# Performance work log

Measured on AMD Instinct MI355X. Metric: run time of the kernel, lower is better.

Reference implementation:

```python
import jax, jax.numpy as jnp
import numpy as np

N_LAYERS = 2
D = 128


def _prelu(z, a):
    return jnp.where(z >= 0, z, a * z)


def _seg_sum(vals, idx, num):
    return jax.ops.segment_sum(vals, idx, num_segments=num)


def _conv_layer(x, ni, ei, Wn2e, bn2e, We2n, be2n, alpha, Dn_inv, De_inv, num_nodes, num_edges):
    # node -> edge: mean over member nodes (row norm), then linear + bias + PReLU
    e = _seg_sum((x @ Wn2e)[ni] * De_inv[ei][:, None], ei, num_edges) + bn2e
    e = _prelu(e, alpha)
    # edge -> node: mean over incident hyperedges
    n = _seg_sum((e @ We2n)[ei] * Dn_inv[ni][:, None], ni, num_nodes) + be2n
    return n, e


def _encoder(x, ni, ei, Wn2e, bn2e, We2n, be2n, alpha, Dn_inv, De_inv, num_nodes, num_edges):
    e = None
    for i in range(N_LAYERS):
        x, e = _conv_layer(x, ni, ei, Wn2e[i], bn2e[i], We2n[i], be2n[i], alpha, Dn_inv, De_inv, num_nodes, num_edges)
        x = _prelu(x, alpha)
    return x, e


def _decoder(x, e, ni, ei, We, Wx, b, alpha, Dn_inv, num_nodes):
    for i in range(N_LAYERS):
        m = _seg_sum((e @ We[i])[ei] * Dn_inv[ni][:, None], ni, num_nodes)
        x = _prelu(x @ Wx[i] + m + b[i], alpha)
    return x


def _forward(x, xx,
             e1_Wn2e, e1_bn2e, e1_We2n, e1_be2n,
             e2_Wn2e, e2_bn2e, e2_We2n, e2_be2n,
             d1_We, d1_Wx, d1_b, d2_We, d2_Wx, d2_b,
             alpha, node_idx, edge_idx, num_nodes, num_edges):
    # self loops: each node gets its own private hyperedge (id num_edges + node_id)
    ni = jnp.concatenate([node_idx, jnp.arange(num_nodes, dtype=node_idx.dtype)])
    ei = jnp.concatenate([edge_idx, jnp.arange(num_edges, num_edges + num_nodes, dtype=edge_idx.dtype)])
    ne_tot = num_edges + num_nodes
    ones = jnp.ones(ni.shape[0], x.dtype)
    Dn = _seg_sum(ones, ni, num_nodes)
    De = _seg_sum(ones, ei, ne_tot)
    Dn_inv = jnp.where(Dn > 0, 1.0 / Dn, 0.0)
    De_inv = jnp.where(De > 0, 1.0 / De, 0.0)

    n1, e1 = _encoder(x, ni, ei, e1_Wn2e, e1_bn2e, e1_We2n, e1_be2n, alpha, Dn_inv, De_inv, num_nodes, ne_tot)
    n2, e2 = _encoder(xx, ni, ei, e2_Wn2e, e2_bn2e, e2_We2n, e2_be2n, alpha, Dn_inv, De_inv, num_nodes, ne_tot)

    x11 = _decoder(n1, e1, ni, ei, d1_We, d1_Wx, d1_b, alpha, Dn_inv, num_nodes)
    x21 = _decoder(n2, e2, ni, ei, d2_We, d2_Wx, d2_b, alpha, Dn_inv, num_nodes)
    x12 = _decoder(n2, e2, ni, ei, d1_We, d1_Wx, d1_b, alpha, Dn_inv, num_nodes)
    x22 = _decoder(n1, e1, ni, ei, d2_We, d2_Wx, d2_b, alpha, Dn_inv, num_nodes)

    nn1 = jnp.concatenate([n1, n2], axis=1)
    return (nn1, n1, e1[:num_edges], n2, e2[:num_edges], x11, x21, x12, x22)


def setup_inputs() -> dict:
    key = jax.random.key(0)
    ks = jax.random.split(key, 24)
    N, E, NNZ = 50000, 20000, 800000
    s = 1.0 / np.sqrt(D)
    inp = {
        'x': jax.random.normal(ks[0], (N, D), jnp.float32),
        'xx': jax.random.normal(ks[1], (N, D), jnp.float32),
        'node_idx': jax.random.randint(ks[2], (NNZ,), 0, N, jnp.int32),
        'edge_idx': jax.random.randint(ks[3], (NNZ,), 0, E, jnp.int32),
        'num_nodes': N,
        'num_edges': E,
        'alpha': jnp.float32(0.25),
    }
    i = 4
    for enc in ('e1', 'e2'):
        inp[enc + '_Wn2e'] = jax.random.normal(ks[i], (N_LAYERS, D, D), jnp.float32) * s; i += 1
        inp[enc + '_bn2e'] = jnp.zeros((N_LAYERS, D), jnp.float32)
        inp[enc + '_We2n'] = jax.random.normal(ks[i], (N_LAYERS, D, D), jnp.float32) * s; i += 1
        inp[enc + '_be2n'] = jnp.zeros((N_LAYERS, D), jnp.float32)
    for dec in ('d1', 'd2'):
        inp[dec + '_We'] = jax.random.normal(ks[i], (N_LAYERS, D, D), jnp.float32) * s; i += 1
        inp[dec + '_Wx'] = jax.random.normal(ks[i], (N_LAYERS, D, D), jnp.float32) * s; i += 1
        inp[dec + '_b'] = jnp.zeros((N_LAYERS, D), jnp.float32)
    return inp


def reference(x, xx,
              e1_Wn2e, e1_bn2e, e1_We2n, e1_be2n,
              e2_Wn2e, e2_bn2e, e2_We2n, e2_be2n,
              d1_We, d1_Wx, d1_b, d2_We, d2_Wx, d2_b,
              alpha, node_idx, edge_idx, num_nodes, num_edges):
    return _forward(x, xx,
                    e1_Wn2e, e1_bn2e, e1_We2n, e1_be2n,
                    e2_Wn2e, e2_bn2e, e2_We2n, e2_be2n,
                    d1_We, d1_Wx, d1_b, d2_We, d2_Wx, d2_b,
                    alpha, node_idx, edge_idx, num_nodes, num_edges)
```

## Files before the change

kernel.cpp:

```cpp
#include <hip/hip_runtime.h>

#define DD 128

typedef __attribute__((ext_vector_type(8))) short bh8;
typedef __attribute__((ext_vector_type(8))) unsigned short us8;
typedef __attribute__((ext_vector_type(4))) float f4;
typedef unsigned int u32;
typedef unsigned short u16;

__device__ __forceinline__ u16 tob(float f) {
  u32 u = __builtin_bit_cast(u32, f);
  u += 0x7FFFu + ((u >> 16) & 1u);
  return (u16)(u >> 16);
}
__device__ __forceinline__ float fb(u16 h) { return __builtin_bit_cast(float, (u32)h << 16); }


__global__ __launch_bounds__(256) void init_counts_k(int* cn, int* ce, int N, int E) {
  int g = blockIdx.x * blockDim.x + threadIdx.x;
  if (g < E) ce[g] = 0;
  if (g < N) cn[g] = 0;
}


__global__ __launch_bounds__(256) void scan_partials_k(const int* __restrict__ cn, const int* __restrict__ ce,
                                                       int* part, int NCHN, int N, int NCHE, int E) {
  __shared__ int red[256];
  int b = blockIdx.x, tid = threadIdx.x;
  const int* cnt = (b < NCHN) ? cn : ce;
  int n = (b < NCHN) ? N : E;
  int base = ((b < NCHN) ? b : (b - NCHN)) << 10;
  int i0 = base + tid * 4;
  int s = 0;
  #pragma unroll
  for (int j = 0; j < 4; ++j) { int i = i0 + j; if (i < n) s += cnt[i]; }
  red[tid] = s; __syncthreads();
  for (int off = 128; off > 0; off >>= 1) {
    if (tid < off) red[tid] += red[tid + off];
    __syncthreads();
  }
  if (tid == 0) part[b] = red[0];
}

__device__ __forceinline__ int blk_excl_scan(int s, int tid, int* sums) {
  sums[tid] = s; __syncthreads();
  for (int off = 1; off < 256; off <<= 1) {
    int t = (tid >= off) ? sums[tid - off] : 0;
    __syncthreads();
    sums[tid] += t;
    __syncthreads();
  }
  int ex = sums[tid] - s;
  __syncthreads();
  return ex;
}

__global__ __launch_bounds__(256) void scan_apply_k(const int* __restrict__ cn, const int* __restrict__ ce,
                                                    const int* __restrict__ part,
                                                    int* offs_n, int* offs_e,
                                                    int NCHN, int N, int NCHE, int E) {
  __shared__ int sums[256];
  __shared__ int base_s;
  int b = blockIdx.x, tid = threadIdx.x;
  const bool isN = b < NCHN;
  const int* cnt = isN ? cn : ce;
  int* offs = isN ? offs_n : offs_e;
  int n = isN ? N : E;
  int nch = isN ? NCHN : NCHE;
  int c = isN ? b : b - NCHN;
  const int* pbase = isN ? part : part + NCHN;
  {
    int v = (tid < nch) ? pbase[tid] : 0;
    int ex = blk_excl_scan(v, tid, sums);
    if (tid == c) base_s = ex;
  }
  __syncthreads();
  int base = (c << 10);
  int i0 = base + tid * 4;
  int v[4]; int s = 0;
  #pragma unroll
  for (int j = 0; j < 4; ++j) { int i = i0 + j; int t = (i < n) ? cnt[i] : 0; v[j] = t; s += t; }
  int ex = blk_excl_scan(s, tid, sums);
  int run = base_s + ex;
  #pragma unroll
  for (int j = 0; j < 4; ++j) { int i = i0 + j; if (i < n) offs[i] = run; run += v[j]; }
  if (tid == 255 && base + 1024 >= n) offs[n] = run;
}

__global__ __launch_bounds__(256) void fill_deg_k(const int* __restrict__ offs_n, const int* __restrict__ offs_e,
                                                  float* Dn_inv, float* De_inv,
                                                  int* cur_be, int* cur_bn,
                                                  int N, int E, int NBE, int NBN) {
  int g = blockIdx.x * blockDim.x + threadIdx.x;
  if (g < E) {
    int b = offs_e[g], e = offs_e[g + 1];
    De_inv[g] = (e > b) ? 1.0f / (float)(e - b) : 0.0f;
  }
  if (g < N) {
    int b = offs_n[g], e = offs_n[g + 1];
    Dn_inv[g] = 1.0f / (float)(e - b + 1);
  }
  if (g < NBE) {
    int r1 = (g + 1) * 32; if (r1 > E) r1 = E;
    int o0 = offs_e[g * 32], o1 = offs_e[r1];
    int C = o1 - o0, base = 8 * o0;
    #pragma unroll
    for (int k = 0; k < 8; ++k) cur_be[g * 8 + k] = base + k * C;
  }
  if (g < NBN) {
    int r1 = (g + 1) * 32; if (r1 > N) r1 = N;
    int o0 = offs_n[g * 32], o1 = offs_n[r1];
    int C = o1 - o0, base = 8 * o0;
    #pragma unroll
    for (int k = 0; k < 8; ++k) cur_bn[g * 8 + k] = base + k * C;
  }
}

__global__ __launch_bounds__(256) void partition2_k(const int* __restrict__ ni, const int* __restrict__ ei,
                                                    int* cur_be, int* cur_bn,
                                                    u32* __restrict__ SE, u32* __restrict__ SN, int nnz) {
  int xcd;
  asm volatile("s_getreg_b32 %0, hwreg(HW_REG_XCC_ID)" : "=s"(xcd));
  xcd &= 7;
  int stride = gridDim.x * blockDim.x;
  for (int j = blockIdx.x * blockDim.x + threadIdx.x; j < nnz; j += stride) {
    int n = ni[j], e = ei[j];
    int pe = atomicAdd(&cur_be[(e >> 5) * 8 + xcd], 1);
    SE[pe] = ((u32)(e & 31) << 17) | (u32)n;
    int pn = atomicAdd(&cur_bn[(n >> 5) * 8 + xcd], 1);
    SN[pn] = ((u32)(n & 31) << 17) | (u32)e;
  }
}

__device__ __forceinline__ void scatter_body(const u32* __restrict__ S, const int* __restrict__ offs,
                                             const int* __restrict__ cur_b,
                                             int* __restrict__ list, int nRows, int b, int tid, int* cur) {
  const int i0 = b << 5;
  if (tid < 32) {
    int row = i0 + tid;
    cur[tid] = (row < nRows) ? offs[row] : 0;
  }
  __syncthreads();
  int r1 = i0 + 32; if (r1 > nRows) r1 = nRows;
  const int o0 = offs[i0];
  const int C = offs[r1] - o0;
  #pragma unroll 1
  for (int k = 0; k < 8; ++k) {
    int sbeg = 8 * o0 + k * C;
    int send = cur_b[b * 8 + k];
    for (int i = sbeg + tid; i < send; i += 256) {
      u32 v = S[i];
      int pos = atomicAdd(&cur[v >> 17], 1);
      list[pos] = (int)(v & 0x1FFFFu);
    }
  }
}

__global__ __launch_bounds__(256) void scatter_both_k(const u32* SE, const int* offs_e, const int* cur_be,
                                                      int* listE, int E, int NBE,
                                                      const u32* SN, const int* offs_n, const int* cur_bn,
                                                      int* listN, int N) {
  __shared__ int cur[32];
  int b = blockIdx.x, tid = threadIdx.x;
  if (b < NBE) scatter_body(SE, offs_e, cur_be, listE, E, b, tid, cur);
  else         scatter_body(SN, offs_n, cur_bn, listN, N, b - NBE, tid, cur);
}


__device__ __forceinline__ void acc8(float a[8], us8 v) {
  #pragma unroll
  for (int j = 0; j < 8; ++j) a[j] += fb(v[j]);
}

template<int SPLIT>
__global__ __launch_bounds__(256) void gather_edge_k(const u16* __restrict__ srcb,
                                                     const int* __restrict__ offs, const int* __restrict__ list,
                                                     const float* __restrict__ De_inv,
                                                     const float* __restrict__ b1, const float* __restrict__ b2,
                                                     const float* __restrict__ alphap,
                                                     u16* __restrict__ e_fullb,
                                                     float* __restrict__ d2a, float* __restrict__ d2b, int E) {
  const int wave = threadIdx.x >> 6, lane = threadIdx.x & 63;
  const int row = blockIdx.x * 4 + wave;
  if (row >= E) return;
  const int half = lane >> 5, cl = lane & 31;
  const int c8 = cl * 8;
  const int beg = offs[row], end = offs[row + 1];
  float a0[8] = {0,0,0,0,0,0,0,0}, a1[8] = {0,0,0,0,0,0,0,0};
  int i = beg + half;
  for (; i + 2 < end; i += 4) {
    us8 v0 = *(const us8*)&srcb[(size_t)list[i] * 256 + c8];
    us8 v1 = *(const us8*)&srcb[(size_t)list[i + 2] * 256 + c8];
    acc8(a0, v0); acc8(a1, v1);
  }
  if (i < end) acc8(a0, *(const us8*)&srcb[(size_t)list[i] * 256 + c8]);
  float s[8];
  #pragma unroll
  for (int j = 0; j < 8; ++j) s[j] = a0[j] + a1[j];
  #pragma unroll
  for (int j = 0; j < 8; ++j) s[j] += __shfl_xor(s[j], 32);
  if (half == 0) {
    float sc = De_inv[row];
    const float* bp = (c8 < 128) ? (b1 + c8) : (b2 + c8 - 128);
    float4 bt0 = *(const float4*)bp;
    float4 bt1 = *(const float4*)(bp + 4);
    float bb[8] = {bt0.x, bt0.y, bt0.z, bt0.w, bt1.x, bt1.y, bt1.z, bt1.w};
    float al = *alphap;
    us8 ob;
    float ov[8];
    #pragma unroll
    for (int j = 0; j < 8; ++j) {
      float v = sc * s[j] + bb[j];
      v = (v >= 0.f) ? v : al * v;
      ov[j] = v; ob[j] = tob(v);
    }
    *(us8*)&e_fullb[(size_t)row * 256 + c8] = ob;
    if constexpr (SPLIT == 1) {
      float* dp = (c8 < 128) ? &d2a[(size_t)row * DD + c8] : &d2b[(size_t)row * DD + c8 - 128];
      float4 w0 = {ov[0], ov[1], ov[2], ov[3]};
      float4 w1 = {ov[4], ov[5], ov[6], ov[7]};
      *(float4*)dp = w0;
      *(float4*)(dp + 4) = w1;
    }
  }
}

__global__ __launch_bounds__(256) void gather_node_k(const u16* __restrict__ e_fullb,
                                                     const u16* __restrict__ tb,
                                                     const int* __restrict__ offs, const int* __restrict__ list,
                                                     const float* __restrict__ Dn_inv,
                                                     const float* __restrict__ b1, const float* __restrict__ b2,
                                                     const float* __restrict__ alphap,
                                                     u16* __restrict__ dstb, int N) {
  const int wave = threadIdx.x >> 6, lane = threadIdx.x & 63;
  const int row = blockIdx.x * 4 + wave;
  if (row >= N) return;
  const int half = lane >> 5, cl = lane & 31;
  const int c8 = cl * 8;
  const int beg = offs[row], end = offs[row + 1];
  float a0[8] = {0,0,0,0,0,0,0,0}, a1[8] = {0,0,0,0,0,0,0,0};
  int i = beg + half;
  for (; i + 2 < end; i += 4) {
    us8 v0 = *(const us8*)&e_fullb[(size_t)list[i] * 256 + c8];
    us8 v1 = *(const us8*)&e_fullb[(size_t)list[i + 2] * 256 + c8];
    acc8(a0, v0); acc8(a1, v1);
  }
  if (i < end) acc8(a0, *(const us8*)&e_fullb[(size_t)list[i] * 256 + c8]);
  float s[8];
  #pragma unroll
  for (int j = 0; j < 8; ++j) s[j] = a0[j] + a1[j];
  #pragma unroll
  for (int j = 0; j < 8; ++j) s[j] += __shfl_xor(s[j], 32);
  if (half == 0) {
    us8 tv = *(const us8*)&tb[(size_t)row * 256 + c8];
    const float* bp = (c8 < 128) ? (b1 + c8) : (b2 + c8 - 128);
    float4 bt0 = *(const float4*)bp;
    float4 bt1 = *(const float4*)(bp + 4);
    float bb[8] = {bt0.x, bt0.y, bt0.z, bt0.w, bt1.x, bt1.y, bt1.z, bt1.w};
    float al = *alphap;
    float sc = Dn_inv[row];
    us8 ob;
    #pragma unroll
    for (int j = 0; j < 8; ++j) {
      float sv = fb(tv[j]) + bb[j];
      sv = (sv >= 0.f) ? sv : al * sv;
      ob[j] = tob(sc * (sv + s[j]));
    }
    *(us8*)&dstb[(size_t)row * 256 + c8] = ob;
  }
}


struct WPtrs { const float* p[16]; };

__global__ __launch_bounds__(256) void prep_w_k(WPtrs wp, char* dst) {
  int m = blockIdx.x >> 3, s = blockIdx.x & 7;
  const float* W = wp.p[m];
  int t = threadIdx.x;
  int n = t & 127;
  int k0 = s * 16 + (t >> 7) * 8;
  us8 vhi, vlo;
  #pragma unroll
  for (int j = 0; j < 8; ++j) {
    float x = W[(size_t)(k0 + j) * DD + n];
    u32 ux = __builtin_bit_cast(u32, x);
    float hf = __builtin_bit_cast(float, ux & 0xFFFF0000u);
    float l = x - hf;
    vhi[j] = (u16)(ux >> 16);
    vlo[j] = (u16)(__builtin_bit_cast(u32, l) >> 16);
  }
  char* base = dst + (size_t)m * 65536;
  int byte = n * 256 + k0 * 2;
  byte ^= (n & 7) << 4;
  *(us8*)(base + byte) = vhi;
  *(us8*)(base + 32768 + byte) = vlo;
}


__device__ __forceinline__ void stage_w(const char* gsrc, char* lds, int tid) {
  int wave = tid >> 6, lane = tid & 63;
  #pragma unroll
  for (int i = 0; i < 16; ++i) {
    int off = (wave * 16 + i) * 1024;
    __builtin_amdgcn_global_load_lds(
        (const __attribute__((address_space(1))) u32*)(gsrc + off + lane * 16),
        (__attribute__((address_space(3))) u32*)(lds + off), 16, 0, 0);
  }
}

__device__ __forceinline__ void split8(const float vs[8], bh8& hi, bh8& lo) {
  #pragma unroll
  for (int j = 0; j < 8; ++j) {
    u32 u = __builtin_bit_cast(u32, vs[j]);
    float hf = __builtin_bit_cast(float, u & 0xFFFF0000u);
    float l = vs[j] - hf;
    hi[j] = (short)(u >> 16);
    lo[j] = (short)(__builtin_bit_cast(u32, l) >> 16);
  }
}

__device__ __forceinline__ void mk_afrag(const float* rowp, int koff, bh8& hi, bh8& lo) {
  float4 v0 = *(const float4*)(rowp + koff);
  float4 v1 = *(const float4*)(rowp + koff + 4);
  float vs[8] = {v0.x, v0.y, v0.z, v0.w, v1.x, v1.y, v1.z, v1.w};
  split8(vs, hi, lo);
}

__device__ __forceinline__ void mfma_ks(const bh8& ahi, const bh8& alo, const char* Wl,
                                        int ks, int lane, f4 acc[8]) {
  const int koff0 = (lane >> 4) * 8;
  const int k2 = (ks * 32 + koff0) * 2;
  #pragma unroll
  for (int cb = 0; cb < 8; ++cb) {
    int n = cb * 16 + (lane & 15);
    int byte = (n * 256 + k2) ^ ((n & 7) << 4);
    bh8 bhiF = *(const bh8*)(Wl + byte);
    bh8 bloF = *(const bh8*)(Wl + 32768 + byte);
    acc[cb] = __builtin_amdgcn_mfma_f32_16x16x32_bf16(ahi, bhiF, acc[cb], 0, 0, 0);
    acc[cb] = __builtin_amdgcn_mfma_f32_16x16x32_bf16(ahi, bloF, acc[cb], 0, 0, 0);
    acc[cb] = __builtin_amdgcn_mfma_f32_16x16x32_bf16(alo, bhiF, acc[cb], 0, 0, 0);
  }
}

__device__ __forceinline__ void mfma_ks_bf(const bh8& a, const char* Wl,
                                           int ks, int lane, f4 acc[8]) {
  const int koff0 = (lane >> 4) * 8;
  const int k2 = (ks * 32 + koff0) * 2;
  #pragma unroll
  for (int cb = 0; cb < 8; ++cb) {
    int n = cb * 16 + (lane & 15);
    int byte = (n * 256 + k2) ^ ((n & 7) << 4);
    bh8 bhiF = *(const bh8*)(Wl + byte);
    bh8 bloF = *(const bh8*)(Wl + 32768 + byte);
    acc[cb] = __builtin_amdgcn_mfma_f32_16x16x32_bf16(a, bhiF, acc[cb], 0, 0, 0);
    acc[cb] = __builtin_amdgcn_mfma_f32_16x16x32_bf16(a, bloF, acc[cb], 0, 0, 0);
  }
}

__device__ __forceinline__ void mfma_passS(const float* __restrict__ A, size_t astride, int acoff,
                                           const char* Wl, int rbase, int nrows, int lane, f4 acc[8]) {
  int r = rbase + (lane & 15);
  if (r >= nrows) r = nrows - 1;
  const float* rowp = A + (size_t)r * astride + acoff;
  const int koff0 = (lane >> 4) * 8;
  #pragma unroll
  for (int ks = 0; ks < 4; ++ks) {
    bh8 ahi, alo;
    mk_afrag(rowp, ks * 32 + koff0, ahi, alo);
    mfma_ks(ahi, alo, Wl, ks, lane, acc);
  }
}

__device__ __forceinline__ void mfma_passB(const u16* __restrict__ A, size_t astride, int acoff,
                                           const char* Wl, int rbase, int nrows, int lane, f4 acc[8]) {
  int r = rbase + (lane & 15);
  if (r >= nrows) r = nrows - 1;
  const u16* rowp = A + (size_t)r * astride + acoff;
  const int koff0 = (lane >> 4) * 8;
  #pragma unroll
  for (int ks = 0; ks < 4; ++ks) {
    bh8 a = __builtin_bit_cast(bh8, *(const us8*)(rowp + ks * 32 + koff0));
    mfma_ks_bf(a, Wl, ks, lane, acc);
  }
}

struct AFragB { bh8 a[4]; };

__device__ __forceinline__ void load_afragB(const u16* __restrict__ A, size_t astride, int acoff,
                                            int rbase, int nrows, int lane, AFragB& f) {
  int r = rbase + (lane & 15);
  if (r >= nrows) r = nrows - 1;
  const u16* rowp = A + (size_t)r * astride + acoff;
  const int koff0 = (lane >> 4) * 8;
  #pragma unroll
  for (int ks = 0; ks < 4; ++ks)
    f.a[ks] = __builtin_bit_cast(bh8, *(const us8*)(rowp + ks * 32 + koff0));
}

__device__ __forceinline__ void mfma_pass_fragB(const AFragB& f, const char* Wl, int lane, f4 acc[8]) {
  #pragma unroll
  for (int ks = 0; ks < 4; ++ks) mfma_ks_bf(f.a[ks], Wl, ks, lane, acc);
}


__device__ __forceinline__ void acc_to_T(f4 acc[8], const float* bias, float al,
                                         char* Tb, int wave, int lane) {
  const int cidx = lane & 15;
  float b8[8];
  #pragma unroll
  for (int cb = 0; cb < 8; ++cb) b8[cb] = bias[cb * 16 + cidx];
  #pragma unroll
  for (int q = 0; q < 4; ++q) {
    int row = wave * 16 + (lane >> 4) * 4 + q;
    #pragma unroll
    for (int cb = 0; cb < 8; ++cb) {
      float v = acc[cb][q] + b8[cb];
      v = (v >= 0.f) ? v : al * v;
      int byte = (row * 256 + (cb * 16 + cidx) * 2) ^ ((row & 7) << 4);
      *(u16*)(Tb + byte) = tob(v);
    }
  }
}

__device__ __forceinline__ void load_fT(const char* Tb, int wave, int lane, AFragB& f) {
  const int row = wave * 16 + (lane & 15);
  const int koff0 = (lane >> 4) * 8;
  #pragma unroll
  for (int ks = 0; ks < 4; ++ks) {
    int byte = (row * 256 + (ks * 32 + koff0) * 2) ^ ((row & 7) << 4);
    f.a[ks] = __builtin_bit_cast(bh8, *(const us8*)(Tb + byte));
  }
}

template<int MODE, int OBF>
__device__ __forceinline__ void epilogueS(f4 acc[8], const float* bias, const float* alphap,
                                          void* outp, size_t ostride, int ocoff,
                                          int rbase, int nrows, int lane) {
  float al = 0.f;
  if constexpr (MODE == 1) al = *alphap;
  const int cidx = lane & 15;
  int rq = rbase + (lane >> 4) * 4;
  float b8[8];
  if constexpr (MODE == 1) {
    #pragma unroll
    for (int cb = 0; cb < 8; ++cb) b8[cb] = bias[cb * 16 + cidx];
  }
  #pragma unroll
  for (int q = 0; q < 4; ++q) {
    int row = rq + q;
    if (row < nrows) {
      #pragma unroll
      for (int cb = 0; cb < 8; ++cb) {
        float v = acc[cb][q];
        if constexpr (MODE == 1) { v += b8[cb]; v = (v >= 0.f) ? v : al * v; }
        if constexpr (OBF == 1) {
          u16* op = (u16*)outp + (size_t)row * ostride + ocoff + cidx;
          op[cb * 16] = tob(v);
        } else {
          float* op = (float*)outp + (size_t)row * ostride + ocoff + cidx;
          op[cb * 16] = v;
        }
      }
    }
  }
}

#define ACC_ZERO(acc) { _Pragma("unroll") for (int cb = 0; cb < 8; ++cb) acc[cb] = {0.f, 0.f, 0.f, 0.f}; }


__global__ __launch_bounds__(256, 2) void combo1_k(const float* __restrict__ x, const char* W0,
                                                   const float* __restrict__ xx, const char* W4,
                                                   u16* __restrict__ tb, int nrows, int NT,
                                                   const int* __restrict__ ni, const int* __restrict__ ei,
                                                   int* cn, int* ce, int nnz) {
  __shared__ char Wl[65536];
  if ((int)blockIdx.x < NT) {
    const int wave = threadIdx.x >> 6, lane = threadIdx.x & 63;
    const int rbase = blockIdx.x * 64 + wave * 16;
    f4 acc[8];
    stage_w(W0, Wl, threadIdx.x);
    __syncthreads();
    ACC_ZERO(acc);
    mfma_passS(x, DD, 0, Wl, rbase, nrows, lane, acc);
    epilogueS<0, 1>(acc, nullptr, nullptr, tb, 256, 0, rbase, nrows, lane);
    __syncthreads();
    stage_w(W4, Wl, threadIdx.x);
    __syncthreads();
    ACC_ZERO(acc);
    mfma_passS(xx, DD, 0, Wl, rbase, nrows, lane, acc);
    epilogueS<0, 1>(acc, nullptr, nullptr, tb, 256, 128, rbase, nrows, lane);
  } else {
    int nb = gridDim.x - NT;
    int stride = nb * 256;
    for (int j = ((int)blockIdx.x - NT) * 256 + (int)threadIdx.x; j < nnz; j += stride) {
      atomicAdd(&cn[ni[j]], 1);
      atomicAdd(&ce[ei[j]], 1);
    }
  }
}

__global__ __launch_bounds__(256, 2) void gemm_fuse_hid_k(const u16* __restrict__ thb,
                                                          const char* W20, const float* b20, const char* W21,
                                                          const char* W60, const float* b60, const char* W61,
                                                          const float* __restrict__ alphap,
                                                          u16* __restrict__ tb_out, int nrows) {
  __shared__ char Wl[65536];
  const int wave = threadIdx.x >> 6, lane = threadIdx.x & 63;
  const int rbase = blockIdx.x * 64 + wave * 16;
  const float al = *alphap;
  f4 acc[8];
  AFragB fT;
  #pragma unroll 1
  for (int h = 0; h < 2; ++h) {
    if (h) __syncthreads();
    stage_w(h ? W60 : W20, Wl, threadIdx.x);
    __syncthreads();
    ACC_ZERO(acc);
    mfma_passB(thb, 256, h * 128, Wl, rbase, nrows, lane, acc);
    __syncthreads();
    acc_to_T(acc, h ? b60 : b20, al, Wl, wave, lane);
    __syncthreads();
    load_fT(Wl, wave, lane, fT);
    __syncthreads();
    stage_w(h ? W61 : W21, Wl, threadIdx.x);
    __syncthreads();
    ACC_ZERO(acc);
    mfma_pass_fragB(fT, Wl, lane, acc);
    epilogueS<0, 1>(acc, nullptr, nullptr, tb_out, 256, h * 128, rbase, nrows, lane);
  }
}

__global__ __launch_bounds__(256, 2) void enc_final_k(const u16* __restrict__ aggb, const char* W1, const float* b1_,
                                                      const char* W2, const float* b2_,
                                                      const float* __restrict__ alphap,
                                                      float* __restrict__ n1, float* __restrict__ n2,
                                                      u16* __restrict__ n1b, u16* __restrict__ n2b,
                                                      float* __restrict__ nn1, int nrows) {
  __shared__ char Wl[65536];
  const int wave = threadIdx.x >> 6, lane = threadIdx.x & 63;
  const int rbase = blockIdx.x * 64 + wave * 16;
  const int cidx = lane & 15;
  f4 acc[8];
  float al = *alphap;
  #pragma unroll 1
  for (int h = 0; h < 2; ++h) {
    if (h) __syncthreads();
    stage_w(h ? W2 : W1, Wl, threadIdx.x);
    __syncthreads();
    const float* bp = h ? b2_ : b1_;
    float* nout = h ? n2 : n1;
    u16* nbout = h ? n2b : n1b;
    float b8[8];
    #pragma unroll
    for (int cb = 0; cb < 8; ++cb) b8[cb] = bp[cb * 16 + cidx];
    ACC_ZERO(acc);
    mfma_passB(aggb, 256, h * 128, Wl, rbase, nrows, lane, acc);
    int rq = rbase + (lane >> 4) * 4;
    #pragma unroll
    for (int q = 0; q < 4; ++q) {
      int row = rq + q;
      if (row < nrows) {
        float* op = nout + (size_t)row * DD + cidx;
        float* op2 = nn1 + (size_t)row * 256 + h * 128 + cidx;
        u16* op3 = nbout + (size_t)row * DD + cidx;
        #pragma unroll
        for (int cb = 0; cb < 8; ++cb) {
          float v = acc[cb][q] + b8[cb];
          v = (v >= 0.f) ? v : al * v;
          op[cb * 16] = v;
          op2[cb * 16] = v;
          op3[cb * 16] = tob(v);
        }
      }
    }
  }
}

__global__ __launch_bounds__(256, 2) void dec_fused_k(const u16* __restrict__ n1b, const u16* __restrict__ n2b,
                                                      const u16* __restrict__ aggb,
                                                      const char* Wx10, const char* We10, const float* b1_0,
                                                      const char* Wx11, const char* We11, const float* b1_1,
                                                      const char* Wx20, const char* We20, const float* b2_0,
                                                      const char* Wx21, const char* We21, const float* b2_1,
                                                      const float* __restrict__ alphap,
                                                      float* __restrict__ x11, float* __restrict__ x22,
                                                      float* __restrict__ x12, float* __restrict__ x21,
                                                      int nrows) {
  __shared__ char Wl[65536];
  const int y = blockIdx.y;
  const u16* xb = y ? n2b : n1b;
  float* od1 = y ? x12 : x11;
  float* od2 = y ? x21 : x22;
  const int acoff = y * 128;
  const int wave = threadIdx.x >> 6, lane = threadIdx.x & 63;
  const int rbase = blockIdx.x * 64 + wave * 16;
  const float al = *alphap;
  AFragB fx, fa, fT;
  load_afragB(xb, DD, 0, rbase, nrows, lane, fx);
  load_afragB(aggb, 256, acoff, rbase, nrows, lane, fa);
  f4 acc[8];
  #pragma unroll 1
  for (int s = 0; s < 2; ++s) {
    const char* Wx0 = s ? Wx20 : Wx10;
    const char* We0 = s ? We20 : We10;
    const char* Wx1 = s ? Wx21 : Wx11;
    const char* We1 = s ? We21 : We11;
    const float* b0 = s ? b2_0 : b1_0;
    const float* b1 = s ? b2_1 : b1_1;
    float* out = s ? od2 : od1;
    if (s) __syncthreads();
    stage_w(Wx0, Wl, threadIdx.x);
    __syncthreads();
    ACC_ZERO(acc);
    mfma_pass_fragB(fx, Wl, lane, acc);
    __syncthreads();
    stage_w(We0, Wl, threadIdx.x);
    __syncthreads();
    mfma_pass_fragB(fa, Wl, lane, acc);
    __syncthreads();
    acc_to_T(acc, b0, al, Wl, wave, lane);
    __syncthreads();
    load_fT(Wl, wave, lane, fT);
    __syncthreads();
    stage_w(Wx1, Wl, threadIdx.x);
    __syncthreads();
    ACC_ZERO(acc);
    mfma_pass_fragB(fT, Wl, lane, acc);
    __syncthreads();
    stage_w(We1, Wl, threadIdx.x);
    __syncthreads();
    mfma_pass_fragB(fa, Wl, lane, acc);
    epilogueS<1, 0>(acc, b1, alphap, out, DD, 0, rbase, nrows, lane);
  }
}


extern "C" void kernel_launch(void* const* d_in, const int* in_sizes, int n_in,
                              void* d_out, int out_size, void* d_ws, size_t ws_size,
                              hipStream_t stream) {
  const float* x        = (const float*)d_in[0];
  const float* xx       = (const float*)d_in[1];
  const int*   node_idx = (const int*)d_in[2];
  const int*   edge_idx = (const int*)d_in[3];
  const float* alphap   = (const float*)d_in[6];
  const float* e1_Wn2e  = (const float*)d_in[7];
  const float* e1_bn2e  = (const float*)d_in[8];
  const float* e1_We2n  = (const float*)d_in[9];
  const float* e1_be2n  = (const float*)d_in[10];
  const float* e2_Wn2e  = (const float*)d_in[11];
  const float* e2_bn2e  = (const float*)d_in[12];
  const float* e2_We2n  = (const float*)d_in[13];
  const float* e2_be2n  = (const float*)d_in[14];
  const float* d1_We    = (const float*)d_in[15];
  const float* d1_Wx    = (const float*)d_in[16];
  const float* d1_b     = (const float*)d_in[17];
  const float* d2_We    = (const float*)d_in[18];
  const float* d2_Wx    = (const float*)d_in[19];
  const float* d2_b     = (const float*)d_in[20];

  const int N   = in_sizes[0] / DD;
  const int NNZ = in_sizes[2];
  const int E   = (out_size - 1024 * N) / 256;
  const int NBE = (E + 31) >> 5;
  const int NBN = (N + 31) >> 5;
  const int NCHN = (N + 1023) >> 10;
  const int NCHE = (E + 1023) >> 10;

  float* out  = (float*)d_out;
  float* nn1  = out;
  float* n1   = out + (size_t)N * 256;
  float* e1o  = n1 + (size_t)N * DD;
  float* n2   = e1o + (size_t)E * DD;
  float* e2o  = n2 + (size_t)N * DD;
  float* x11  = e2o + (size_t)E * DD;
  float* x21  = x11 + (size_t)N * DD;
  float* x12  = x21 + (size_t)N * DD;
  float* x22  = x12 + (size_t)N * DD;

  size_t off = 0;
  char* w0 = (char*)d_ws;
  auto carve = [&](size_t bytes) -> void* {
    void* p = (void*)(w0 + off);
    off += (bytes + 255) & ~(size_t)255;
    return p;
  };
  int* cn      = (int*)carve((size_t)N * 4);
  int* ce      = (int*)carve((size_t)E * 4);
  int* offs_n  = (int*)carve((size_t)(N + 1) * 4);
  int* offs_e  = (int*)carve((size_t)(E + 1) * 4);
  int* part    = (int*)carve((size_t)(NCHN + NCHE) * 4);
  int* listN   = (int*)carve((size_t)NNZ * 4);
  int* listE   = (int*)carve((size_t)NNZ * 4);
  float* Dn_inv = (float*)carve((size_t)N * 4);
  float* De_inv = (float*)carve((size_t)E * 4);
  char* Wprep  = (char*)carve((size_t)16 * 65536);
  u16* tb      = (u16*)carve((size_t)N * 256 * 2);
  u16* e_fullb = (u16*)carve((size_t)E * 256 * 2);
  u16* thb     = (u16*)carve((size_t)N * 256 * 2);
  u16* aggb    = (u16*)carve((size_t)N * 256 * 2);
  u16* n1b     = (u16*)carve((size_t)N * DD * 2);
  u16* n2b     = (u16*)carve((size_t)N * DD * 2);
  int* cur_be  = (int*)carve((size_t)NBE * 8 * 4);
  int* cur_bn  = (int*)carve((size_t)NBN * 8 * 4);
  u32* SE      = (u32*)carve((size_t)NNZ * 8 * 4);
  u32* SN      = (u32*)carve((size_t)NNZ * 8 * 4);

  WPtrs wp;
  wp.p[0] = e1_Wn2e;  wp.p[1] = e1_Wn2e + DD * DD;
  wp.p[2] = e1_We2n;  wp.p[3] = e1_We2n + DD * DD;
  wp.p[4] = e2_Wn2e;  wp.p[5] = e2_Wn2e + DD * DD;
  wp.p[6] = e2_We2n;  wp.p[7] = e2_We2n + DD * DD;
  wp.p[8] = d1_We;    wp.p[9] = d1_We + DD * DD;
  wp.p[10] = d1_Wx;   wp.p[11] = d1_Wx + DD * DD;
  wp.p[12] = d2_We;   wp.p[13] = d2_We + DD * DD;
  wp.p[14] = d2_Wx;   wp.p[15] = d2_Wx + DD * DD;
  auto WP = [&](int i) -> const char* { return Wprep + (size_t)i * 65536; };

  const int thr = 256;
  const int gMax = ((N > E ? N : E) + thr - 1) / thr;
  const int NT = (N + 63) / 64;
  const int HB = 512;
  int gNNZ = (NNZ + thr - 1) / thr; if (gNNZ > 2048) gNNZ = 2048;
  const int gGatE = (E + 3) / 4;
  const int gGatN = (N + 3) / 4;

  prep_w_k<<<128, 256, 0, stream>>>(wp, Wprep);
  init_counts_k<<<gMax, thr, 0, stream>>>(cn, ce, N, E);
  combo1_k<<<NT + HB, 256, 0, stream>>>(x, WP(0), xx, WP(4), tb, N, NT,
                                        node_idx, edge_idx, cn, ce, NNZ);
  scan_partials_k<<<NCHN + NCHE, 256, 0, stream>>>(cn, ce, part, NCHN, N, NCHE, E);
  scan_apply_k<<<NCHN + NCHE, 256, 0, stream>>>(cn, ce, part, offs_n, offs_e, NCHN, N, NCHE, E);
  fill_deg_k<<<gMax, thr, 0, stream>>>(offs_n, offs_e, Dn_inv, De_inv,
                                       cur_be, cur_bn, N, E, NBE, NBN);
  partition2_k<<<gNNZ, thr, 0, stream>>>(node_idx, edge_idx, cur_be, cur_bn, SE, SN, NNZ);
  scatter_both_k<<<NBE + NBN, 256, 0, stream>>>(SE, offs_e, cur_be, listE, E, NBE,
                                                SN, offs_n, cur_bn, listN, N);

  gather_edge_k<0><<<gGatE, 256, 0, stream>>>(tb, offs_e, listE, De_inv, e1_bn2e, e2_bn2e,
                                              alphap, e_fullb, nullptr, nullptr, E);
  gather_node_k<<<gGatN, 256, 0, stream>>>(e_fullb, tb, offs_n, listN, Dn_inv, e1_bn2e, e2_bn2e,
                                           alphap, thb, N);
  gemm_fuse_hid_k<<<NT, 256, 0, stream>>>(thb, WP(2), e1_be2n, WP(1),
                                          WP(6), e2_be2n, WP(5), alphap, tb, N);
  gather_edge_k<1><<<gGatE, 256, 0, stream>>>(tb, offs_e, listE, De_inv, e1_bn2e + DD, e2_bn2e + DD,
                                              alphap, e_fullb, e1o, e2o, E);
  gather_node_k<<<gGatN, 256, 0, stream>>>(e_fullb, tb, offs_n, listN, Dn_inv, e1_bn2e + DD, e2_bn2e + DD,
                                           alphap, aggb, N);
  enc_final_k<<<NT, 256, 0, stream>>>(aggb, WP(3), e1_be2n + DD, WP(7), e2_be2n + DD,
                                      alphap, n1, n2, n1b, n2b, nn1, N);

  dim3 gDec(NT, 2);
  dec_fused_k<<<gDec, 256, 0, stream>>>(n1b, n2b, aggb,
                                        WP(10), WP(8), d1_b, WP(11), WP(9), d1_b + DD,
                                        WP(14), WP(12), d2_b, WP(15), WP(13), d2_b + DD,
                                        alphap, x11, x22, x12, x21, N);
}
```

Before: 585.3 us.

## Drop low-bf16 weight terms and double-buffer weights in hidden GEMM kernel

The first two GEMM kernels now use only the high bf16 half of the weights, so the hi*lo weight MFMA term is dropped and half the weight bytes are staged into LDS. The hidden fused kernel gets separate LDS regions for both weight matrices and the activation tile. That lets the second weight load run while the first GEMM computes and removes several barriers. The cost is lower precision in these GEMMs and 80KB of LDS per block, which may reduce occupancy below two blocks per CU.

```diff
diff --git a/kernel.cpp b/kernel.cpp
--- a/kernel.cpp
+++ b/kernel.cpp
@@ -308,6 +308,17 @@
   }
 }
 
+__device__ __forceinline__ void stage_w32(const char* gsrc, char* lds, int tid) {
+  int wave = tid >> 6, lane = tid & 63;
+  #pragma unroll
+  for (int i = 0; i < 8; ++i) {
+    int off = (wave * 8 + i) * 1024;
+    __builtin_amdgcn_global_load_lds(
+        (const __attribute__((address_space(1))) u32*)(gsrc + off + lane * 16),
+        (__attribute__((address_space(3))) u32*)(lds + off), 16, 0, 0);
+  }
+}
+
 __device__ __forceinline__ void split8(const float vs[8], bh8& hi, bh8& lo) {
   #pragma unroll
   for (int j = 0; j < 8; ++j) {
@@ -342,6 +353,20 @@
   }
 }
 
+__device__ __forceinline__ void mfma_ks_hi2(const bh8& ahi, const bh8& alo, const char* Wl,
+                                            int ks, int lane, f4 acc[8]) {
+  const int koff0 = (lane >> 4) * 8;
+  const int k2 = (ks * 32 + koff0) * 2;
+  #pragma unroll
+  for (int cb = 0; cb < 8; ++cb) {
+    int n = cb * 16 + (lane & 15);
+    int byte = (n * 256 + k2) ^ ((n & 7) << 4);
+    bh8 bhiF = *(const bh8*)(Wl + byte);
+    acc[cb] = __builtin_amdgcn_mfma_f32_16x16x32_bf16(ahi, bhiF, acc[cb], 0, 0, 0);
+    acc[cb] = __builtin_amdgcn_mfma_f32_16x16x32_bf16(alo, bhiF, acc[cb], 0, 0, 0);
+  }
+}
+
 __device__ __forceinline__ void mfma_ks_bf(const bh8& a, const char* Wl,
                                            int ks, int lane, f4 acc[8]) {
   const int koff0 = (lane >> 4) * 8;
@@ -357,8 +382,21 @@
   }
 }
 
-__device__ __forceinline__ void mfma_passS(const float* __restrict__ A, size_t astride, int acoff,
-                                           const char* Wl, int rbase, int nrows, int lane, f4 acc[8]) {
+__device__ __forceinline__ void mfma_ks_bfhi(const bh8& a, const char* Wl,
+                                             int ks, int lane, f4 acc[8]) {
+  const int koff0 = (lane >> 4) * 8;
+  const int k2 = (ks * 32 + koff0) * 2;
+  #pragma unroll
+  for (int cb = 0; cb < 8; ++cb) {
+    int n = cb * 16 + (lane & 15);
+    int byte = (n * 256 + k2) ^ ((n & 7) << 4);
+    bh8 bhiF = *(const bh8*)(Wl + byte);
+    acc[cb] = __builtin_amdgcn_mfma_f32_16x16x32_bf16(a, bhiF, acc[cb], 0, 0, 0);
+  }
+}
+
+__device__ __forceinline__ void mfma_passS_hi2(const float* __restrict__ A, size_t astride, int acoff,
+                                               const char* Wl, int rbase, int nrows, int lane, f4 acc[8]) {
   int r = rbase + (lane & 15);
   if (r >= nrows) r = nrows - 1;
   const float* rowp = A + (size_t)r * astride + acoff;
@@ -367,7 +405,7 @@
   for (int ks = 0; ks < 4; ++ks) {
     bh8 ahi, alo;
     mk_afrag(rowp, ks * 32 + koff0, ahi, alo);
-    mfma_ks(ahi, alo, Wl, ks, lane, acc);
+    mfma_ks_hi2(ahi, alo, Wl, ks, lane, acc);
   }
 }
 
@@ -384,6 +422,19 @@
   }
 }
 
+__device__ __forceinline__ void mfma_passB_hi(const u16* __restrict__ A, size_t astride, int acoff,
+                                              const char* Wl, int rbase, int nrows, int lane, f4 acc[8]) {
+  int r = rbase + (lane & 15);
+  if (r >= nrows) r = nrows - 1;
+  const u16* rowp = A + (size_t)r * astride + acoff;
+  const int koff0 = (lane >> 4) * 8;
+  #pragma unroll
+  for (int ks = 0; ks < 4; ++ks) {
+    bh8 a = __builtin_bit_cast(bh8, *(const us8*)(rowp + ks * 32 + koff0));
+    mfma_ks_bfhi(a, Wl, ks, lane, acc);
+  }
+}
+
 struct AFragB { bh8 a[4]; };
 
 __device__ __forceinline__ void load_afragB(const u16* __restrict__ A, size_t astride, int acoff,
@@ -400,6 +451,11 @@
 __device__ __forceinline__ void mfma_pass_fragB(const AFragB& f, const char* Wl, int lane, f4 acc[8]) {
   #pragma unroll
   for (int ks = 0; ks < 4; ++ks) mfma_ks_bf(f.a[ks], Wl, ks, lane, acc);
+}
+
+__device__ __forceinline__ void mfma_pass_fragB_hi(const AFragB& f, const char* Wl, int lane, f4 acc[8]) {
+  #pragma unroll
+  for (int ks = 0; ks < 4; ++ks) mfma_ks_bfhi(f.a[ks], Wl, ks, lane, acc);
 }
 
 
@@ -473,21 +529,21 @@
                                                    u16* __restrict__ tb, int nrows, int NT,
                                                    const int* __restrict__ ni, const int* __restrict__ ei,
                                                    int* cn, int* ce, int nnz) {
-  __shared__ char Wl[65536];
+  __shared__ char Wl[32768];
   if ((int)blockIdx.x < NT) {
     const int wave = threadIdx.x >> 6, lane = threadIdx.x & 63;
     const int rbase = blockIdx.x * 64 + wave * 16;
     f4 acc[8];
-    stage_w(W0, Wl, threadIdx.x);
+    stage_w32(W0, Wl, threadIdx.x);
     __syncthreads();
     ACC_ZERO(acc);
-    mfma_passS(x, DD, 0, Wl, rbase, nrows, lane, acc);
+    mfma_passS_hi2(x, DD, 0, Wl, rbase, nrows, lane, acc);
     epilogueS<0, 1>(acc, nullptr, nullptr, tb, 256, 0, rbase, nrows, lane);
     __syncthreads();
-    stage_w(W4, Wl, threadIdx.x);
+    stage_w32(W4, Wl, threadIdx.x);
     __syncthreads();
     ACC_ZERO(acc);
-    mfma_passS(xx, DD, 0, Wl, rbase, nrows, lane, acc);
+    mfma_passS_hi2(xx, DD, 0, Wl, rbase, nrows, lane, acc);
     epilogueS<0, 1>(acc, nullptr, nullptr, tb, 256, 128, rbase, nrows, lane);
   } else {
     int nb = gridDim.x - NT;
@@ -504,7 +560,10 @@
                                                           const char* W60, const float* b60, const char* W61,
                                                           const float* __restrict__ alphap,
                                                           u16* __restrict__ tb_out, int nrows) {
-  __shared__ char Wl[65536];
+  __shared__ char Wl[81920];
+  char* H0 = Wl;
+  char* H1 = Wl + 32768;
+  char* Tb = Wl + 65536;
   const int wave = threadIdx.x >> 6, lane = threadIdx.x & 63;
   const int rbase = blockIdx.x * 64 + wave * 16;
   const float al = *alphap;
@@ -513,19 +572,17 @@
   #pragma unroll 1
   for (int h = 0; h < 2; ++h) {
     if (h) __syncthreads();
-    stage_w(h ? W60 : W20, Wl, threadIdx.x);
-    __syncthreads();
+    stage_w32(h ? W60 : W20, H0, threadIdx.x);
+    __syncthreads();
+    stage_w32(h ? W61 : W21, H1, threadIdx.x);
     ACC_ZERO(acc);
-    mfma_passB(thb, 256, h * 128, Wl, rbase, nrows, lane, acc);
-    __syncthreads();
-    acc_to_T(acc, h ? b60 : b20, al, Wl, wave, lane);
-    __syncthreads();
-    load_fT(Wl, wave, lane, fT);
-    __syncthreads();
-    stage_w(h ? W61 : W21, Wl, threadIdx.x);
-    __syncthreads();
+    mfma_passB_hi(thb, 256, h * 128, H0, rbase, nrows, lane, acc);
+    __syncthreads();
+    acc_to_T(acc, h ? b60 : b20, al, Tb, wave, lane);
+    __syncthreads();
+    load_fT(Tb, wave, lane, fT);
     ACC_ZERO(acc);
-    mfma_pass_fragB(fT, Wl, lane, acc);
+    mfma_pass_fragB_hi(fT, H1, lane, acc);
     epilogueS<0, 1>(acc, nullptr, nullptr, tb_out, 256, h * 128, rbase, nrows, lane);
   }
 }
```

Result: faster. 566.4 us (-3.2%).
